# Performance work log

Measured on AMD Instinct MI355X. Metric: run time of the kernel, lower is better.

The kernel has to match this reference:

```python
import jax, jax.numpy as jnp
import numpy as np

B, N, C, H, HD, HH, WW, K, ALPHA = 8, 4096, 256, 8, 32, 64, 64, 5, 4.0


def setup_inputs() -> dict:
    key = jax.random.key(0)
    ks = jax.random.split(key, 6)
    return {
        "x": jax.random.normal(ks[0], (B, N, C), jnp.float32),
        "W_qg": jax.random.normal(ks[1], (C, 2 * C), jnp.float32) * 0.02,
        "W_kv": jax.random.normal(ks[2], (C, 2 * C), jnp.float32) * 0.02,
        "W_proj": jax.random.normal(ks[3], (C, C), jnp.float32) * 0.02,
        "b_proj": jnp.zeros((C,), jnp.float32),
        "dwc_w": jax.random.normal(ks[4], (HD, 1, K, K), jnp.float32) * 0.05,
        "dwc_b": jnp.zeros((HD,), jnp.float32),
        "power_p": jnp.zeros((1, H, 1, HD), jnp.float32),
    }


def _safe_pow(x, p):
    # x >= 0 (post-relu). 0**p == 0 for p > 0; guard base so grads stay finite.
    xs = jnp.where(x > 0, x, 1.0)
    return jnp.where(x > 0, xs ** p, 0.0)


def reference(x, W_qg, W_kv, W_proj, b_proj, dwc_w, dwc_b, power_p):
    qg = x @ W_qg                                  # (B,N,2C)
    q, g = qg[..., :C], qg[..., C:]
    kv = x @ W_kv                                  # (B,N,2C)
    k = kv[..., :C].reshape(B, N, H, HD).transpose(0, 2, 1, 3)   # (B,H,N,hd)
    v = kv[..., C:].reshape(B, N, H, HD).transpose(0, 2, 1, 3)
    q = q.reshape(B, N, H, HD).transpose(0, 2, 1, 3)

    power = 1.0 + ALPHA * jax.nn.sigmoid(power_p)  # (1,H,1,hd)
    # x_s = q_pos@kv_s + q_neg@kv_s = (q_pos+q_neg)@kv_s, kv_s = (k_pos+k_neg)^T v_s
    q_sum = _safe_pow(jax.nn.relu(q), power) + _safe_pow(jax.nn.relu(-q), power)
    k_sum = _safe_pow(jax.nn.relu(k), power) + _safe_pow(jax.nn.relu(-k), power)

    v_s, v_o = v[..., : HD // 2], v[..., HD // 2 :]
    kv_s = jnp.einsum('bhnd,bhne->bhde', k_sum, v_s)
    kv_o = jnp.einsum('bhnd,bhne->bhde', k_sum, v_o)
    x_s = jnp.einsum('bhnd,bhde->bhne', q_sum, kv_s)
    x_o = jnp.einsum('bhnd,bhde->bhne', q_sum, kv_o)
    x_att = jnp.concatenate([x_s, x_o], -1).transpose(0, 2, 1, 3).reshape(B, N, C)

    # depthwise conv branch: exact layout replication of torch permute/reshape chain
    v_img = v.transpose(0, 2, 1, 3).reshape(B * H, HD, HH, WW)
    pad = K // 2
    v_loc = jax.lax.conv_general_dilated(
        v_img, dwc_w, (1, 1), [(pad, pad), (pad, pad)],
        feature_group_count=HD,
        dimension_numbers=('NCHW', 'OIHW', 'NCHW')) + dwc_b[None, :, None, None]
    v_loc = v_loc.reshape(B, H, HD, N).transpose(0, 2, 1, 3).reshape(B, C, N).transpose(0, 2, 1)

    return ((x_att + v_loc) * g) @ W_proj + b_proj
```

## Files before the change

kernel.cpp:

```cpp
#include <hip/hip_runtime.h>
#include <hip/hip_bf16.h>
#include <math.h>

#define B_ 8
#define N_ 4096
#define C_ 256
#define H_ 8
#define HD_ 32
#define BN_ (B_ * N_)
#define E_ ((size_t)BN_ * C_)

typedef __attribute__((ext_vector_type(8))) short short8;
typedef __attribute__((ext_vector_type(4))) float f32x4;

__device__ __forceinline__ float b2f(__hip_bfloat16 x) { return __bfloat162float(x); }

__device__ __forceinline__ void gl_lds16(const void* gp, void* lp) {
    __builtin_amdgcn_global_load_lds(
        (const __attribute__((address_space(1))) unsigned int*)gp,
        (__attribute__((address_space(3))) unsigned int*)lp,
        16, 0, 0);
}

__device__ __forceinline__ float fast_abspow(float v, float p) {
    float av = fabsf(v);
    return (av > 0.f) ? __builtin_amdgcn_exp2f(p * __builtin_amdgcn_logf(av)) : 0.f;
}

__device__ __forceinline__ float bf_lo(unsigned u) { return __uint_as_float(u << 16); }
__device__ __forceinline__ float bf_hi(unsigned u) { return __uint_as_float(u & 0xffff0000u); }
__device__ __forceinline__ unsigned short f2bfbits(float f) {
    __hip_bfloat16 h = __float2bfloat16(f);
    return *(unsigned short*)&h;
}
__device__ __forceinline__ unsigned pack2(float lo, float hi) {
    return (unsigned)f2bfbits(lo) | ((unsigned)f2bfbits(hi) << 16);
}

__global__ __launch_bounds__(256) void cvt_all(
    const float* __restrict__ x, const float* __restrict__ Wqg,
    const float* __restrict__ Wkv, const float* __restrict__ Wp,
    const float* __restrict__ pp,
    __hip_bfloat16* __restrict__ xb, __hip_bfloat16* __restrict__ Wt1,
    __hip_bfloat16* __restrict__ Wt2, float* __restrict__ powers)
{
    int t = threadIdx.x;
    int bid0 = blockIdx.x;
    if (bid0 < 4096) {
        size_t i = ((size_t)bid0 * 256 + t) * 8;
        float4 a = *(const float4*)&x[i];
        float4 b = *(const float4*)&x[i + 4];
        uint4 o = {pack2(a.x, a.y), pack2(a.z, a.w), pack2(b.x, b.y), pack2(b.z, b.w)};
        *(uint4*)&xb[i] = o;
        return;
    }
    int bid = bid0 - 4096;
    if (bid == 80) {
        powers[t] = 1.0f + 4.0f / (1.0f + expf(-pp[t]));
        return;
    }
    __shared__ float tile[64][65];
    const float* src;
    __hip_bfloat16* dst;
    int scols, tr, tc, dn0;
    if (bid < 32)      { src = Wqg; scols = 512; tr = bid >> 3;        tc = bid & 7;        dst = Wt1; dn0 = tc * 64; }
    else if (bid < 64) { src = Wkv; scols = 512; tr = (bid - 32) >> 3; tc = (bid - 32) & 7; dst = Wt1; dn0 = 512 + tc * 64; }
    else               { src = Wp;  scols = 256; tr = (bid - 64) >> 2; tc = (bid - 64) & 3; dst = Wt2; dn0 = tc * 64; }
    int tx = t & 63, ty = t >> 6;
    #pragma unroll
    for (int i = 0; i < 16; i++) {
        int r = ty + i * 4;
        tile[r][tx] = src[(size_t)(tr * 64 + r) * scols + tc * 64 + tx];
    }
    __syncthreads();
    #pragma unroll
    for (int i = 0; i < 16; i++) {
        int n_local = ty + i * 4;
        dst[(size_t)(dn0 + n_local) * 256 + tr * 64 + tx] = __float2bfloat16(tile[tx][n_local]);
    }
}

__global__ __launch_bounds__(256) void gemm1_mfma(
    const __hip_bfloat16* __restrict__ xb, const __hip_bfloat16* __restrict__ Wt1,
    const float* __restrict__ powers,
    __hip_bfloat16* __restrict__ q16, __hip_bfloat16* __restrict__ k16,
    __hip_bfloat16* __restrict__ g16, __hip_bfloat16* __restrict__ v16)
{
    __shared__ __align__(16) unsigned short As[2 * 128 * 32];
    __shared__ __align__(16) unsigned short Bs[2 * 128 * 32];
    int t = threadIdx.x;
    int w = t >> 6, l = t & 63;
    int bswz = (blockIdx.x & 7) * 256 + (blockIdx.x >> 3);
    int row0 = (bswz >> 3) * 128;
    int colb = bswz & 7;
    int col0 = colb * 128;
    int wm = (w >> 1) * 64, wn = (w & 1) * 64;
    int lane15 = l & 15, quad = l >> 4;
    int srow = l >> 2;
    int skcol = (l & 3) * 8;

    f32x4 acc[4][4];
    #pragma unroll
    for (int mi = 0; mi < 4; mi++)
        #pragma unroll
        for (int ni = 0; ni < 4; ni++) acc[mi][ni] = (f32x4){0.f, 0.f, 0.f, 0.f};

    for (int k0 = 0; k0 < 256; k0 += 64) {
        #pragma unroll
        for (int kh = 0; kh < 2; kh++) {
            #pragma unroll
            for (int i = 0; i < 2; i++) {
                int r = i * 64 + w * 16 + srow;
                int kc = k0 + kh * 32 + skcol;
                gl_lds16(&xb[(size_t)(row0 + r) * 256 + kc],
                         &As[kh * 4096 + (i * 64 + w * 16) * 32]);
                gl_lds16(&Wt1[(size_t)(col0 + r) * 256 + kc],
                         &Bs[kh * 4096 + (i * 64 + w * 16) * 32]);
            }
        }
        __syncthreads();
        #pragma unroll
        for (int kh = 0; kh < 2; kh++) {
            short8 a[4], b[4];
            #pragma unroll
            for (int mi = 0; mi < 4; mi++)
                a[mi] = *(const short8*)&As[kh * 4096 + (wm + mi * 16 + lane15) * 32 + quad * 8];
            #pragma unroll
            for (int ni = 0; ni < 4; ni++)
                b[ni] = *(const short8*)&Bs[kh * 4096 + (wn + ni * 16 + lane15) * 32 + quad * 8];
            #pragma unroll
            for (int mi = 0; mi < 4; mi++)
                #pragma unroll
                for (int ni = 0; ni < 4; ni++)
                    acc[mi][ni] = __builtin_amdgcn_mfma_f32_16x16x32_bf16(a[mi], b[ni], acc[mi][ni], 0, 0, 0);
        }
        __syncthreads();
    }

    int region = colb >> 1;
    bool dopow = (region == 0) || (region == 2);
    __hip_bfloat16* dst = (region == 0) ? q16 : (region == 1) ? g16 : (region == 2) ? k16 : v16;
    #pragma unroll
    for (int mi = 0; mi < 4; mi++) {
        #pragma unroll
        for (int ni = 0; ni < 4; ni++) {
            int row = row0 + wm + mi * 16 + quad * 4;
            int col = col0 + wn + ni * 16 + lane15;
            int c255 = col & 255;
            float p = powers[c255];
            #pragma unroll
            for (int r = 0; r < 4; r++) {
                float v = acc[mi][ni][r];
                float o = dopow ? fast_abspow(v, p) : v;
                dst[(size_t)(row + r) * 256 + c255] = __float2bfloat16(o);
            }
        }
    }
}

__global__ __launch_bounds__(256) void kvmat_kernel(
    const __hip_bfloat16* __restrict__ k16, const __hip_bfloat16* __restrict__ v16,
    float* __restrict__ kv_part)
{
    __shared__ __align__(16) unsigned short Kl[16 * 256];
    __shared__ __align__(16) unsigned short Vl[16 * 256];
    int t = threadIdx.x;
    int bid = blockIdx.x;
    int b = bid >> 6, seg = bid & 63;
    int h = t >> 5;
    float acc[32];
    #pragma unroll
    for (int e = 0; e < 32; e++) acc[e] = 0.f;
    const size_t base = (size_t)b * N_ * 256;
    int row = t >> 4, colb = (t & 15) * 16;
    for (int n0 = seg * 64; n0 < seg * 64 + 64; n0 += 16) {
        const uint4* ks = (const uint4*)(k16 + base + (size_t)(n0 + row) * 256 + colb);
        uint4 ka = ks[0], kb = ks[1];
        const uint4* vs = (const uint4*)(v16 + base + (size_t)(n0 + row) * 256 + colb);
        uint4 va = vs[0], vb = vs[1];
        __syncthreads();
        uint4* kd4 = (uint4*)&Kl[row * 256 + colb];
        kd4[0] = ka; kd4[1] = kb;
        uint4* vd4 = (uint4*)&Vl[row * 256 + colb];
        vd4[0] = va; vd4[1] = vb;
        __syncthreads();
        #pragma unroll
        for (int nn = 0; nn < 16; nn++) {
            float kd = bf_lo((unsigned)Kl[nn * 256 + t]);
            const uint4* vp = (const uint4*)&Vl[nn * 256 + h * 32];
            uint4 v0 = vp[0], v1 = vp[1], v2 = vp[2], v3 = vp[3];
            unsigned us[16] = {v0.x, v0.y, v0.z, v0.w, v1.x, v1.y, v1.z, v1.w,
                               v2.x, v2.y, v2.z, v2.w, v3.x, v3.y, v3.z, v3.w};
            #pragma unroll
            for (int j = 0; j < 16; j++) {
                acc[2 * j]     += kd * bf_lo(us[j]);
                acc[2 * j + 1] += kd * bf_hi(us[j]);
            }
        }
    }
    float* dst = kv_part + (size_t)bid * 8192;
    #pragma unroll
    for (int e = 0; e < 32; e++) dst[e * 256 + t] = acc[e];
}

__global__ __launch_bounds__(256) void kv_reduce(
    const float* __restrict__ kv_part, float* __restrict__ kv_mat2)
{
    int bid = blockIdx.x, t = threadIdx.x;
    int b = bid >> 5, chunk = bid & 31;
    int i = chunk * 256 + t;
    float s = 0.f;
    for (int seg = 0; seg < 64; seg++)
        s += kv_part[((size_t)b * 64 + seg) * 8192 + i];
    kv_mat2[(size_t)b * 8192 + i] = s;
}

__global__ __launch_bounds__(256) void conv_kernel(
    const __hip_bfloat16* __restrict__ v16,
    const float* __restrict__ w, const float* __restrict__ bias,
    __hip_bfloat16* __restrict__ vloc)
{
    __shared__ __align__(16) float img[64 * 72];
    __shared__ float wl[25];
    int t = threadIdx.x;
    int gid = blockIdx.x;
    int DD = gid & 31;
    if (t < 128) {
        int row = t >> 1, side = (t & 1) * 68;
        *(float4*)&img[row * 72 + side] = (float4){0.f, 0.f, 0.f, 0.f};
    }
    if (t < 25) wl[t] = w[DD * 25 + t];
    {
        int row = t >> 2, colb = (t & 3) * 16;
        const uint4* src = (const uint4*)(v16 + (size_t)gid * 4096 + row * 64 + colb);
        uint4 u0 = src[0], u1 = src[1];
        float4* d = (float4*)&img[row * 72 + 4 + colb];
        d[0] = (float4){bf_lo(u0.x), bf_hi(u0.x), bf_lo(u0.y), bf_hi(u0.y)};
        d[1] = (float4){bf_lo(u0.z), bf_hi(u0.z), bf_lo(u0.w), bf_hi(u0.w)};
        d[2] = (float4){bf_lo(u1.x), bf_hi(u1.x), bf_lo(u1.y), bf_hi(u1.y)};
        d[3] = (float4){bf_lo(u1.z), bf_hi(u1.z), bf_lo(u1.w), bf_hi(u1.w)};
    }
    __syncthreads();
    float bs = bias[DD];
    int x0 = (t & 15) * 4, yb = t >> 4;
    #pragma unroll
    for (int s = 0; s < 4; s++) {
        int y = yb + s * 16;
        float a0 = bs, a1 = bs, a2 = bs, a3 = bs;
        #pragma unroll
        for (int ky = 0; ky < 5; ky++) {
            int row = y + ky - 2;
            if (row < 0 || row >= 64) continue;
            const float* rp = &img[row * 72 + x0];
            float4 w0 = *(const float4*)rp;
            float4 w1 = *(const float4*)(rp + 4);
            float4 w2 = *(const float4*)(rp + 8);
            float win[12] = {w0.x, w0.y, w0.z, w0.w, w1.x, w1.y, w1.z, w1.w,
                             w2.x, w2.y, w2.z, w2.w};
            #pragma unroll
            for (int kx = 0; kx < 5; kx++) {
                float wt = wl[ky * 5 + kx];
                a0 += wt * win[2 + kx];
                a1 += wt * win[3 + kx];
                a2 += wt * win[4 + kx];
                a3 += wt * win[5 + kx];
            }
        }
        unsigned lo = pack2(a0, a1);
        unsigned hi = pack2(a2, a3);
        *(uint2*)(vloc + (size_t)gid * 4096 + y * 64 + x0) = (uint2){lo, hi};
    }
}

#define A2P 264
__global__ __launch_bounds__(256) void att_gemm2(
    const __hip_bfloat16* __restrict__ q16, const float* __restrict__ kv_mat2,
    const __hip_bfloat16* __restrict__ vloc, const __hip_bfloat16* __restrict__ g16,
    const __hip_bfloat16* __restrict__ Wt2, const float* __restrict__ bp,
    float* __restrict__ out)
{
    __shared__ __align__(16) unsigned short QA[64 * A2P];
    __shared__ __align__(16) unsigned short Bs[256 * 32];
    int t = threadIdx.x;
    int w = t >> 6, l = t & 63;
    int r0 = blockIdx.x * 64;
    int b = r0 >> 12, n0 = r0 & 4095;
    int lane15 = l & 15, quad = l >> 4;
    int h0 = w * 2;

    {
        const uint4* qsrc = (const uint4*)(q16 + (size_t)(r0 + (t >> 2)) * 256 + (t & 3) * 64);
        uint4* qdst = (uint4*)&QA[(t >> 2) * A2P + (t & 3) * 64];
        #pragma unroll
        for (int j = 0; j < 8; j++) qdst[j] = qsrc[j];
    }
    __syncthreads();

    short8 afr[4][2];
    #pragma unroll
    for (int m = 0; m < 4; m++)
        #pragma unroll
        for (int hh = 0; hh < 2; hh++)
            afr[m][hh] = *(const short8*)&QA[(m * 16 + lane15) * A2P + (h0 + hh) * 32 + quad * 8];

    short8 bfr[2][2];
    #pragma unroll
    for (int hh = 0; hh < 2; hh++) {
        #pragma unroll
        for (int nt = 0; nt < 2; nt++) {
            const float4* kp = (const float4*)(kv_mat2 + (size_t)b * 8192 +
                (size_t)(nt * 16 + lane15) * 256 + (h0 + hh) * 32 + quad * 8);
            float4 ka = kp[0], kb = kp[1];
            short8 bb;
            bb[0] = (short)f2bfbits(ka.x); bb[1] = (short)f2bfbits(ka.y);
            bb[2] = (short)f2bfbits(ka.z); bb[3] = (short)f2bfbits(ka.w);
            bb[4] = (short)f2bfbits(kb.x); bb[5] = (short)f2bfbits(kb.y);
            bb[6] = (short)f2bfbits(kb.z); bb[7] = (short)f2bfbits(kb.w);
            bfr[hh][nt] = bb;
        }
    }

    f32x4 ac[4][2][2];
    #pragma unroll
    for (int m = 0; m < 4; m++)
        #pragma unroll
        for (int hh = 0; hh < 2; hh++)
            #pragma unroll
            for (int nt = 0; nt < 2; nt++)
                ac[m][hh][nt] = __builtin_amdgcn_mfma_f32_16x16x32_bf16(
                    afr[m][hh], bfr[hh][nt], (f32x4){0.f, 0.f, 0.f, 0.f}, 0, 0, 0);

    #pragma unroll
    for (int m = 0; m < 4; m++) {
        #pragma unroll
        for (int hh = 0; hh < 2; hh++) {
            #pragma unroll
            for (int nt = 0; nt < 2; nt++) {
                int col = (h0 + hh) * 32 + nt * 16 + lane15;
                int rowb = m * 16 + quad * 4;
                size_t img = ((size_t)((b * 8 + (col & 7)) * 32 + (col >> 3))) * 4096 + n0 + rowb;
                uint2 vv = *(const uint2*)(vloc + img);
                float vl[4] = {bf_lo(vv.x), bf_hi(vv.x), bf_lo(vv.y), bf_hi(vv.y)};
                #pragma unroll
                for (int i = 0; i < 4; i++) {
                    float gg = b2f(g16[(size_t)(r0 + rowb + i) * 256 + col]);
                    float val = (ac[m][hh][nt][i] + vl[i]) * gg;
                    QA[(rowb + i) * A2P + col] = f2bfbits(val);
                }
            }
        }
    }

    int wm = (w & 1) * 32, wn = (w >> 1) * 128;
    f32x4 acc2[2][8];
    #pragma unroll
    for (int mi = 0; mi < 2; mi++)
        #pragma unroll
        for (int ni = 0; ni < 8; ni++) acc2[mi][ni] = (f32x4){0.f, 0.f, 0.f, 0.f};

    for (int k0 = 0; k0 < 256; k0 += 32) {
        __syncthreads();
        #pragma unroll
        for (int i = 0; i < 4; i++) {
            int ncol = i * 64 + w * 16 + (l >> 2);
            gl_lds16(&Wt2[(size_t)ncol * 256 + k0 + (l & 3) * 8],
                     &Bs[(i * 64 + w * 16) * 32]);
        }
        __syncthreads();
        short8 a[2], bb[8];
        #pragma unroll
        for (int mi = 0; mi < 2; mi++)
            a[mi] = *(const short8*)&QA[(wm + mi * 16 + lane15) * A2P + k0 + quad * 8];
        #pragma unroll
        for (int ni = 0; ni < 8; ni++)
            bb[ni] = *(const short8*)&Bs[(wn + ni * 16 + lane15) * 32 + quad * 8];
        #pragma unroll
        for (int mi = 0; mi < 2; mi++)
            #pragma unroll
            for (int ni = 0; ni < 8; ni++)
                acc2[mi][ni] = __builtin_amdgcn_mfma_f32_16x16x32_bf16(a[mi], bb[ni], acc2[mi][ni], 0, 0, 0);
    }

    #pragma unroll
    for (int mi = 0; mi < 2; mi++) {
        #pragma unroll
        for (int ni = 0; ni < 8; ni++) {
            int row = r0 + wm + mi * 16 + quad * 4;
            int col = wn + ni * 16 + lane15;
            float bv = bp[col];
            #pragma unroll
            for (int r = 0; r < 4; r++)
                out[(size_t)(row + r) * 256 + col] = acc2[mi][ni][r] + bv;
        }
    }
}

extern "C" void kernel_launch(void* const* d_in, const int* in_sizes, int n_in,
                              void* d_out, int out_size, void* d_ws, size_t ws_size,
                              hipStream_t stream) {
    const float* x      = (const float*)d_in[0];
    const float* W_qg   = (const float*)d_in[1];
    const float* W_kv   = (const float*)d_in[2];
    const float* W_proj = (const float*)d_in[3];
    const float* b_proj = (const float*)d_in[4];
    const float* dwc_w  = (const float*)d_in[5];
    const float* dwc_b  = (const float*)d_in[6];
    const float* pow_p  = (const float*)d_in[7];
    float* out = (float*)d_out;

    float* ws = (float*)d_ws;
    const size_t E = E_;
    __hip_bfloat16* q16  = (__hip_bfloat16*)ws;
    __hip_bfloat16* k16  = (__hip_bfloat16*)(ws + E / 2);
    __hip_bfloat16* g16  = (__hip_bfloat16*)(ws + E);
    __hip_bfloat16* v16  = (__hip_bfloat16*)(ws + 3 * E / 2);
    __hip_bfloat16* xb   = (__hip_bfloat16*)(ws + 2 * E);
    __hip_bfloat16* vl16 = (__hip_bfloat16*)(ws + 5 * E / 2);
    float* kv_part = ws + 2 * E;
    float* kv_mat2 = ws + 3 * E + 256 * 8192;
    __hip_bfloat16* Wt1 = (__hip_bfloat16*)(kv_mat2 + 65536);
    __hip_bfloat16* Wt2 = Wt1 + 262144;
    float* powers = (float*)(Wt2 + 65536);

    cvt_all<<<4096 + 81, 256, 0, stream>>>(x, W_qg, W_kv, W_proj, pow_p, xb, Wt1, Wt2, powers);
    gemm1_mfma<<<2048, 256, 0, stream>>>(xb, Wt1, powers, q16, k16, g16, v16);
    kvmat_kernel<<<512, 256, 0, stream>>>(k16, v16, kv_part);
    kv_reduce<<<256, 256, 0, stream>>>(kv_part, kv_mat2);
    conv_kernel<<<2048, 256, 0, stream>>>(v16, dwc_w, dwc_b, vl16);
    att_gemm2<<<512, 256, 0, stream>>>(q16, kv_mat2, vl16, g16, Wt2, b_proj, out);
}
```

Before: 203.4 us.

## Load GEMM operands directly from global memory and store conv output token-major

Both GEMM kernels now read MFMA operand fragments straight from global memory into registers instead of staging them through LDS with global_load_lds and barriers. gemm1 also switches to 128x256 tiles per block with 4x8 accumulators, halves the grid, and adds an occupancy hint of 2. The conv kernel writes its output in (B,N,C) token-major layout so att_gemm2 can read it row-wise alongside g16. The intent is to cut LDS traffic and synchronisation; the cost is uncoalesced 16-byte global reads that rely on cache reuse, heavier register pressure, and scattered 2-byte stores in conv.

Measured after the change: 266.8 us. +31.2%, slower.

```diff
diff --git a/kernel.cpp b/kernel.cpp
--- a/kernel.cpp
+++ b/kernel.cpp
@@ -80,79 +80,60 @@
     }
 }
 
-__global__ __launch_bounds__(256) void gemm1_mfma(
+__global__ __launch_bounds__(256, 2) void gemm1_mfma(
     const __hip_bfloat16* __restrict__ xb, const __hip_bfloat16* __restrict__ Wt1,
     const float* __restrict__ powers,
     __hip_bfloat16* __restrict__ q16, __hip_bfloat16* __restrict__ k16,
     __hip_bfloat16* __restrict__ g16, __hip_bfloat16* __restrict__ v16)
 {
-    __shared__ __align__(16) unsigned short As[2 * 128 * 32];
-    __shared__ __align__(16) unsigned short Bs[2 * 128 * 32];
     int t = threadIdx.x;
     int w = t >> 6, l = t & 63;
-    int bswz = (blockIdx.x & 7) * 256 + (blockIdx.x >> 3);
-    int row0 = (bswz >> 3) * 128;
-    int colb = bswz & 7;
-    int col0 = colb * 128;
-    int wm = (w >> 1) * 64, wn = (w & 1) * 64;
+    int bswz = (blockIdx.x & 7) * 128 + (blockIdx.x >> 3);
+    int row0 = (bswz >> 2) * 128;
+    int cp = bswz & 3;
+    int col0 = cp * 256;
+    int wm = (w & 1) * 64, wn = (w >> 1) * 128;
     int lane15 = l & 15, quad = l >> 4;
-    int srow = l >> 2;
-    int skcol = (l & 3) * 8;
-
-    f32x4 acc[4][4];
+
+    const __hip_bfloat16* Arow = xb  + (size_t)(row0 + wm + lane15) * 256 + quad * 8;
+    const __hip_bfloat16* Brow = Wt1 + (size_t)(col0 + wn + lane15) * 256 + quad * 8;
+
+    f32x4 acc[4][8];
     #pragma unroll
     for (int mi = 0; mi < 4; mi++)
         #pragma unroll
-        for (int ni = 0; ni < 4; ni++) acc[mi][ni] = (f32x4){0.f, 0.f, 0.f, 0.f};
-
-    for (int k0 = 0; k0 < 256; k0 += 64) {
-        #pragma unroll
-        for (int kh = 0; kh < 2; kh++) {
-            #pragma unroll
-            for (int i = 0; i < 2; i++) {
-                int r = i * 64 + w * 16 + srow;
-                int kc = k0 + kh * 32 + skcol;
-                gl_lds16(&xb[(size_t)(row0 + r) * 256 + kc],
-                         &As[kh * 4096 + (i * 64 + w * 16) * 32]);
-                gl_lds16(&Wt1[(size_t)(col0 + r) * 256 + kc],
-                         &Bs[kh * 4096 + (i * 64 + w * 16) * 32]);
-            }
-        }
-        __syncthreads();
-        #pragma unroll
-        for (int kh = 0; kh < 2; kh++) {
-            short8 a[4], b[4];
-            #pragma unroll
-            for (int mi = 0; mi < 4; mi++)
-                a[mi] = *(const short8*)&As[kh * 4096 + (wm + mi * 16 + lane15) * 32 + quad * 8];
-            #pragma unroll
-            for (int ni = 0; ni < 4; ni++)
-                b[ni] = *(const short8*)&Bs[kh * 4096 + (wn + ni * 16 + lane15) * 32 + quad * 8];
-            #pragma unroll
-            for (int mi = 0; mi < 4; mi++)
-                #pragma unroll
-                for (int ni = 0; ni < 4; ni++)
-                    acc[mi][ni] = __builtin_amdgcn_mfma_f32_16x16x32_bf16(a[mi], b[ni], acc[mi][ni], 0, 0, 0);
-        }
-        __syncthreads();
-    }
-
-    int region = colb >> 1;
-    bool dopow = (region == 0) || (region == 2);
-    __hip_bfloat16* dst = (region == 0) ? q16 : (region == 1) ? g16 : (region == 2) ? k16 : v16;
+        for (int ni = 0; ni < 8; ni++) acc[mi][ni] = (f32x4){0.f, 0.f, 0.f, 0.f};
+
+    #pragma unroll
+    for (int ks = 0; ks < 8; ks++) {
+        short8 a[4], b[8];
+        #pragma unroll
+        for (int mi = 0; mi < 4; mi++)
+            a[mi] = *(const short8*)(Arow + (size_t)mi * 16 * 256 + ks * 32);
+        #pragma unroll
+        for (int ni = 0; ni < 8; ni++)
+            b[ni] = *(const short8*)(Brow + (size_t)ni * 16 * 256 + ks * 32);
+        #pragma unroll
+        for (int mi = 0; mi < 4; mi++)
+            #pragma unroll
+            for (int ni = 0; ni < 8; ni++)
+                acc[mi][ni] = __builtin_amdgcn_mfma_f32_16x16x32_bf16(a[mi], b[ni], acc[mi][ni], 0, 0, 0);
+    }
+
+    bool dopow = (cp == 0) || (cp == 2);
+    __hip_bfloat16* dst = (cp == 0) ? q16 : (cp == 1) ? g16 : (cp == 2) ? k16 : v16;
     #pragma unroll
     for (int mi = 0; mi < 4; mi++) {
         #pragma unroll
-        for (int ni = 0; ni < 4; ni++) {
+        for (int ni = 0; ni < 8; ni++) {
             int row = row0 + wm + mi * 16 + quad * 4;
-            int col = col0 + wn + ni * 16 + lane15;
-            int c255 = col & 255;
-            float p = powers[c255];
+            int col = wn + ni * 16 + lane15;
+            float p = powers[col];
             #pragma unroll
             for (int r = 0; r < 4; r++) {
                 float v = acc[mi][ni][r];
                 float o = dopow ? fast_abspow(v, p) : v;
-                dst[(size_t)(row + r) * 256 + c255] = __float2bfloat16(o);
+                dst[(size_t)(row + r) * 256 + col] = __float2bfloat16(o);
             }
         }
     }
@@ -225,6 +206,9 @@
     int t = threadIdx.x;
     int gid = blockIdx.x;
     int DD = gid & 31;
+    int bb_ = gid >> 8;
+    int pidx = gid & 255;
+    int ocol = (pidx & 31) * 8 + (pidx >> 5);
     if (t < 128) {
         int row = t >> 1, side = (t & 1) * 68;
         *(float4*)&img[row * 72 + side] = (float4){0.f, 0.f, 0.f, 0.f};
@@ -266,9 +250,11 @@
                 a3 += wt * win[5 + kx];
             }
         }
-        unsigned lo = pack2(a0, a1);
-        unsigned hi = pack2(a2, a3);
-        *(uint2*)(vloc + (size_t)gid * 4096 + y * 64 + x0) = (uint2){lo, hi};
+        size_t nb = ((size_t)(bb_ * 4096 + y * 64 + x0)) * 256 + ocol;
+        vloc[nb]           = __float2bfloat16(a0);
+        vloc[nb + 256]     = __float2bfloat16(a1);
+        vloc[nb + 512]     = __float2bfloat16(a2);
+        vloc[nb + 768]     = __float2bfloat16(a3);
     }
 }
 
@@ -280,11 +266,10 @@
     float* __restrict__ out)
 {
     __shared__ __align__(16) unsigned short QA[64 * A2P];
-    __shared__ __align__(16) unsigned short Bs[256 * 32];
     int t = threadIdx.x;
     int w = t >> 6, l = t & 63;
     int r0 = blockIdx.x * 64;
-    int b = r0 >> 12, n0 = r0 & 4095;
+    int b = r0 >> 12;
     int lane15 = l & 15, quad = l >> 4;
     int h0 = w * 2;
 
@@ -338,42 +323,35 @@
             for (int nt = 0; nt < 2; nt++) {
                 int col = (h0 + hh) * 32 + nt * 16 + lane15;
                 int rowb = m * 16 + quad * 4;
-                size_t img = ((size_t)((b * 8 + (col & 7)) * 32 + (col >> 3))) * 4096 + n0 + rowb;
-                uint2 vv = *(const uint2*)(vloc + img);
-                float vl[4] = {bf_lo(vv.x), bf_hi(vv.x), bf_lo(vv.y), bf_hi(vv.y)};
                 #pragma unroll
                 for (int i = 0; i < 4; i++) {
+                    float vl = b2f(vloc[(size_t)(r0 + rowb + i) * 256 + col]);
                     float gg = b2f(g16[(size_t)(r0 + rowb + i) * 256 + col]);
-                    float val = (ac[m][hh][nt][i] + vl[i]) * gg;
+                    float val = (ac[m][hh][nt][i] + vl) * gg;
                     QA[(rowb + i) * A2P + col] = f2bfbits(val);
                 }
             }
         }
     }
+    __syncthreads();
 
     int wm = (w & 1) * 32, wn = (w >> 1) * 128;
+    const __hip_bfloat16* Brow = Wt2 + (size_t)(wn + lane15) * 256 + quad * 8;
     f32x4 acc2[2][8];
     #pragma unroll
     for (int mi = 0; mi < 2; mi++)
         #pragma unroll
         for (int ni = 0; ni < 8; ni++) acc2[mi][ni] = (f32x4){0.f, 0.f, 0.f, 0.f};
 
-    for (int k0 = 0; k0 < 256; k0 += 32) {
-        __syncthreads();
-        #pragma unroll
-        for (int i = 0; i < 4; i++) {
-            int ncol = i * 64 + w * 16 + (l >> 2);
-            gl_lds16(&Wt2[(size_t)ncol * 256 + k0 + (l & 3) * 8],
-                     &Bs[(i * 64 + w * 16) * 32]);
-        }
-        __syncthreads();
+    #pragma unroll
+    for (int ks = 0; ks < 8; ks++) {
         short8 a[2], bb[8];
         #pragma unroll
         for (int mi = 0; mi < 2; mi++)
-            a[mi] = *(const short8*)&QA[(wm + mi * 16 + lane15) * A2P + k0 + quad * 8];
+            a[mi] = *(const short8*)&QA[(wm + mi * 16 + lane15) * A2P + ks * 32 + quad * 8];
         #pragma unroll
         for (int ni = 0; ni < 8; ni++)
-            bb[ni] = *(const short8*)&Bs[(wn + ni * 16 + lane15) * 32 + quad * 8];
+            bb[ni] = *(const short8*)(Brow + (size_t)ni * 16 * 256 + ks * 32);
         #pragma unroll
         for (int mi = 0; mi < 2; mi++)
             #pragma unroll
@@ -423,7 +401,7 @@
     float* powers = (float*)(Wt2 + 65536);
 
     cvt_all<<<4096 + 81, 256, 0, stream>>>(x, W_qg, W_kv, W_proj, pow_p, xb, Wt1, Wt2, powers);
-    gemm1_mfma<<<2048, 256, 0, stream>>>(xb, Wt1, powers, q16, k16, g16, v16);
+    gemm1_mfma<<<1024, 256, 0, stream>>>(xb, Wt1, powers, q16, k16, g16, v16);
     kvmat_kernel<<<512, 256, 0, stream>>>(k16, v16, kv_part);
     kv_reduce<<<256, 256, 0, stream>>>(kv_part, kv_mat2);
     conv_kernel<<<2048, 256, 0, stream>>>(v16, dwc_w, dwc_b, vl16);
```

## Fuse x bf16 conversion into GEMM1 and replace kv reduce with atomics

Applied to the files above, without the earlier changes.

The separate pass that converts x to bf16 is removed. GEMM1 now loads fp32 x directly, packs it to bf16 and writes it to LDS, which saves a full write and read of the bf16 copy of x. The kv partial-sum buffer and its reduce kernel are replaced by float atomicAdd into kv_mat2, which cvt_all zeroes first. This drops one launch and the partial traffic. The cost is that the A operand no longer uses async global-to-LDS loads, fp32 reads are twice as wide, and atomics make the summation order nondeterministic.

Result: slower. 224.4 us (+10.3%).

```diff
diff --git a/kernel.cpp b/kernel.cpp
--- a/kernel.cpp
+++ b/kernel.cpp
@@ -38,25 +38,19 @@
 }
 
 __global__ __launch_bounds__(256) void cvt_all(
-    const float* __restrict__ x, const float* __restrict__ Wqg,
-    const float* __restrict__ Wkv, const float* __restrict__ Wp,
-    const float* __restrict__ pp,
-    __hip_bfloat16* __restrict__ xb, __hip_bfloat16* __restrict__ Wt1,
-    __hip_bfloat16* __restrict__ Wt2, float* __restrict__ powers)
+    const float* __restrict__ Wqg, const float* __restrict__ Wkv,
+    const float* __restrict__ Wp, const float* __restrict__ pp,
+    __hip_bfloat16* __restrict__ Wt1, __hip_bfloat16* __restrict__ Wt2,
+    float* __restrict__ powers, float* __restrict__ kv_mat2)
 {
     int t = threadIdx.x;
-    int bid0 = blockIdx.x;
-    if (bid0 < 4096) {
-        size_t i = ((size_t)bid0 * 256 + t) * 8;
-        float4 a = *(const float4*)&x[i];
-        float4 b = *(const float4*)&x[i + 4];
-        uint4 o = {pack2(a.x, a.y), pack2(a.z, a.w), pack2(b.x, b.y), pack2(b.z, b.w)};
-        *(uint4*)&xb[i] = o;
-        return;
-    }
-    int bid = bid0 - 4096;
+    int bid = blockIdx.x;
     if (bid == 80) {
         powers[t] = 1.0f + 4.0f / (1.0f + expf(-pp[t]));
+        return;
+    }
+    if (bid >= 81) {
+        ((float4*)kv_mat2)[(size_t)(bid - 81) * 256 + t] = (float4){0.f, 0.f, 0.f, 0.f};
         return;
     }
     __shared__ float tile[64][65];
@@ -81,7 +75,7 @@
 }
 
 __global__ __launch_bounds__(256) void gemm1_mfma(
-    const __hip_bfloat16* __restrict__ xb, const __hip_bfloat16* __restrict__ Wt1,
+    const float* __restrict__ x, const __hip_bfloat16* __restrict__ Wt1,
     const float* __restrict__ powers,
     __hip_bfloat16* __restrict__ q16, __hip_bfloat16* __restrict__ k16,
     __hip_bfloat16* __restrict__ g16, __hip_bfloat16* __restrict__ v16)
@@ -98,6 +92,8 @@
     int lane15 = l & 15, quad = l >> 4;
     int srow = l >> 2;
     int skcol = (l & 3) * 8;
+    int arow = t >> 1;
+    int acol = (t & 1) * 16;
 
     f32x4 acc[4][4];
     #pragma unroll
@@ -112,11 +108,21 @@
             for (int i = 0; i < 2; i++) {
                 int r = i * 64 + w * 16 + srow;
                 int kc = k0 + kh * 32 + skcol;
-                gl_lds16(&xb[(size_t)(row0 + r) * 256 + kc],
-                         &As[kh * 4096 + (i * 64 + w * 16) * 32]);
                 gl_lds16(&Wt1[(size_t)(col0 + r) * 256 + kc],
                          &Bs[kh * 4096 + (i * 64 + w * 16) * 32]);
             }
+        }
+        #pragma unroll
+        for (int kh = 0; kh < 2; kh++) {
+            const float* src = &x[(size_t)(row0 + arow) * 256 + k0 + kh * 32 + acol];
+            float4 f0 = *(const float4*)(src);
+            float4 f1 = *(const float4*)(src + 4);
+            float4 f2 = *(const float4*)(src + 8);
+            float4 f3 = *(const float4*)(src + 12);
+            uint4 o0 = {pack2(f0.x, f0.y), pack2(f0.z, f0.w), pack2(f1.x, f1.y), pack2(f1.z, f1.w)};
+            uint4 o1 = {pack2(f2.x, f2.y), pack2(f2.z, f2.w), pack2(f3.x, f3.y), pack2(f3.z, f3.w)};
+            uint4* dst4 = (uint4*)&As[kh * 4096 + arow * 32 + acol];
+            dst4[0] = o0; dst4[1] = o1;
         }
         __syncthreads();
         #pragma unroll
@@ -160,7 +166,7 @@
 
 __global__ __launch_bounds__(256) void kvmat_kernel(
     const __hip_bfloat16* __restrict__ k16, const __hip_bfloat16* __restrict__ v16,
-    float* __restrict__ kv_part)
+    float* __restrict__ kv_mat2)
 {
     __shared__ __align__(16) unsigned short Kl[16 * 256];
     __shared__ __align__(16) unsigned short Vl[16 * 256];
@@ -198,21 +204,9 @@
             }
         }
     }
-    float* dst = kv_part + (size_t)bid * 8192;
-    #pragma unroll
-    for (int e = 0; e < 32; e++) dst[e * 256 + t] = acc[e];
-}
-
-__global__ __launch_bounds__(256) void kv_reduce(
-    const float* __restrict__ kv_part, float* __restrict__ kv_mat2)
-{
-    int bid = blockIdx.x, t = threadIdx.x;
-    int b = bid >> 5, chunk = bid & 31;
-    int i = chunk * 256 + t;
-    float s = 0.f;
-    for (int seg = 0; seg < 64; seg++)
-        s += kv_part[((size_t)b * 64 + seg) * 8192 + i];
-    kv_mat2[(size_t)b * 8192 + i] = s;
+    float* dst = kv_mat2 + (size_t)b * 8192;
+    #pragma unroll
+    for (int e = 0; e < 32; e++) atomicAdd(&dst[e * 256 + t], acc[e]);
 }
 
 __global__ __launch_bounds__(256) void conv_kernel(
@@ -414,18 +408,15 @@
     __hip_bfloat16* k16  = (__hip_bfloat16*)(ws + E / 2);
     __hip_bfloat16* g16  = (__hip_bfloat16*)(ws + E);
     __hip_bfloat16* v16  = (__hip_bfloat16*)(ws + 3 * E / 2);
-    __hip_bfloat16* xb   = (__hip_bfloat16*)(ws + 2 * E);
-    __hip_bfloat16* vl16 = (__hip_bfloat16*)(ws + 5 * E / 2);
-    float* kv_part = ws + 2 * E;
-    float* kv_mat2 = ws + 3 * E + 256 * 8192;
+    __hip_bfloat16* vl16 = (__hip_bfloat16*)(ws + 2 * E);
+    float* kv_mat2 = ws + 5 * E / 2;
     __hip_bfloat16* Wt1 = (__hip_bfloat16*)(kv_mat2 + 65536);
     __hip_bfloat16* Wt2 = Wt1 + 262144;
     float* powers = (float*)(Wt2 + 65536);
 
-    cvt_all<<<4096 + 81, 256, 0, stream>>>(x, W_qg, W_kv, W_proj, pow_p, xb, Wt1, Wt2, powers);
-    gemm1_mfma<<<2048, 256, 0, stream>>>(xb, Wt1, powers, q16, k16, g16, v16);
-    kvmat_kernel<<<512, 256, 0, stream>>>(k16, v16, kv_part);
-    kv_reduce<<<256, 256, 0, stream>>>(kv_part, kv_mat2);
+    cvt_all<<<145, 256, 0, stream>>>(W_qg, W_kv, W_proj, pow_p, Wt1, Wt2, powers, kv_mat2);
+    gemm1_mfma<<<2048, 256, 0, stream>>>(x, Wt1, powers, q16, k16, g16, v16);
+    kvmat_kernel<<<512, 256, 0, stream>>>(k16, v16, kv_mat2);
     conv_kernel<<<2048, 256, 0, stream>>>(v16, dwc_w, dwc_b, vl16);
     att_gemm2<<<512, 256, 0, stream>>>(q16, kv_mat2, vl16, g16, Wt2, b_proj, out);
 }
```
